# Kernel tuning notes

Hardware: AMD Instinct MI355X
Metric: run time of the kernel (lower is better)

Reference implementation:

```python
import jax, jax.numpy as jnp
import numpy as np
import math

EMB = 512

def setup_inputs() -> dict:
    key = jax.random.key(0)
    ks = jax.random.split(key, 7)
    B, L, E = 4, 4096, EMB
    s = 1.0 / math.sqrt(E)
    return {
        "x": jax.random.normal(ks[0], (B, L, E), dtype=jnp.float32),
        "Wq": jax.random.normal(ks[1], (E, E), dtype=jnp.float32) * s,
        "bq": jax.random.normal(ks[2], (E,), dtype=jnp.float32) * 0.01,
        "Wk": jax.random.normal(ks[3], (E, E), dtype=jnp.float32) * s,
        "bk": jax.random.normal(ks[4], (E,), dtype=jnp.float32) * 0.01,
        "Wv": jax.random.normal(ks[5], (E, E), dtype=jnp.float32) * s,
        "bv": jax.random.normal(ks[6], (E,), dtype=jnp.float32) * 0.01,
    }

def reference(x, Wq, bq, Wk, bk, Wv, bv):
    # x: [B, L, E]; Linear weights stored torch-style [out, in]
    E = x.shape[-1]
    L = x.shape[1]
    q = jnp.einsum('ble,fe->blf', x, Wq) + bq
    k = jnp.einsum('ble,fe->blf', x, Wk) + bk
    v = jnp.einsum('ble,fe->blf', x, Wv) + bv
    qk = jnp.einsum('bqe,bke->bqk', q, k)  # [B, L, L]
    # causal mask: strict upper triangle filled with -1e9 BEFORE scaling (as in source)
    mask = jnp.triu(jnp.ones((L, L), dtype=bool), k=1)
    qk = jnp.where(mask, jnp.float32(-1e9), qk)
    att = jax.nn.softmax(qk / jnp.sqrt(jnp.float32(E)), axis=-1)
    return jnp.einsum('bqk,bke->bqe', att, v)
```

## Files before the change

### kernel.cpp

```cpp
#include <hip/hip_runtime.h>

typedef unsigned short u16;
typedef unsigned int u32;
typedef short bf16x8 __attribute__((ext_vector_type(8)));
typedef float f32x4 __attribute__((ext_vector_type(4)));
typedef u16 u16x8 __attribute__((ext_vector_type(8)));
typedef u16 u16x4 __attribute__((ext_vector_type(4)));

typedef const __attribute__((address_space(1))) u32* gas_ptr;
typedef __attribute__((address_space(3))) u32* las_ptr;

#define LQ   4096
#define EMB  512
#define NB   4
#define MROWS (NB * LQ)
#define QSCALE 0.04419417382415922f

__device__ __forceinline__ u16 f2bf(float f) {
  unsigned u = __builtin_bit_cast(unsigned, f);
  u += 0x7fffu + ((u >> 16) & 1u);
  return (u16)(u >> 16);
}
__device__ __forceinline__ float bf2f(u16 h) {
  unsigned u = ((unsigned)h) << 16;
  return __builtin_bit_cast(float, u);
}

__global__ void prep_w(const float* __restrict__ Wq, const float* __restrict__ bq,
                       const float* __restrict__ Wk, const float* __restrict__ bk,
                       const float* __restrict__ Wv, const float* __restrict__ bv,
                       u16* __restrict__ wqb, u16* __restrict__ wkb, u16* __restrict__ wvb,
                       float* __restrict__ bias) {
  int i = blockIdx.x * 256 + threadIdx.x;
  if (i < EMB * EMB) {
    wqb[i] = f2bf(Wq[i] * QSCALE);
    wkb[i] = f2bf(Wk[i]);
    wvb[i] = f2bf(Wv[i]);
  }
  if (i < EMB) {
    bias[i]           = bq[i] * QSCALE;
    bias[EMB + i]     = bk[i];
    bias[2 * EMB + i] = bv[i];
  }
}

__global__ void prep_x(const float* __restrict__ x, u16* __restrict__ xb) {
  int i = blockIdx.x * 256 + threadIdx.x;
  const float4* p = (const float4*)(x + (size_t)i * 8);
  float4 a = p[0], b = p[1];
  u16x8 o;
  o[0] = f2bf(a.x); o[1] = f2bf(a.y); o[2] = f2bf(a.z); o[3] = f2bf(a.w);
  o[4] = f2bf(b.x); o[5] = f2bf(b.y); o[6] = f2bf(b.z); o[7] = f2bf(b.w);
  *(u16x8*)(xb + (size_t)i * 8) = o;
}

__device__ __forceinline__ void gemm_tile_core(
    const u16* __restrict__ A, int lda,
    const u16* __restrict__ B, int ldb,
    int kIters, u16* ldsA, u16* ldsB,
    f32x4 acc[4][4], int tid, int lane, int wr, int wc)
{
  int wave = tid >> 6;
  for (int kb = 0; kb < kIters; ++kb) {
    const u16* ga = A + kb * 64;
    const u16* gb = B + kb * 64;
#pragma unroll
    for (int p = 0; p < 4; ++p) {
      int c = tid + p * 256;
      int row = c >> 3, hh = c & 7;
      int h = hh ^ (row & 7);
      const u16* sa = ga + (size_t)row * lda + h * 8;
      const u16* sb = gb + (size_t)row * ldb + h * 8;
      u16* la = ldsA + wave * 512 + p * 2048;
      u16* lb = ldsB + wave * 512 + p * 2048;
      __builtin_amdgcn_global_load_lds((gas_ptr)(const void*)sa, (las_ptr)(void*)la, 16, 0, 0);
      __builtin_amdgcn_global_load_lds((gas_ptr)(const void*)sb, (las_ptr)(void*)lb, 16, 0, 0);
    }
    __syncthreads();
#pragma unroll
    for (int s = 0; s < 2; ++s) {
      bf16x8 af[4], bfr[4];
#pragma unroll
      for (int m = 0; m < 4; ++m) {
        int row = wr * 64 + m * 16 + (lane & 15);
        int hh = (s * 4 + (lane >> 4)) ^ (row & 7);
        af[m] = *(const bf16x8*)(ldsA + row * 64 + hh * 8);
      }
#pragma unroll
      for (int n = 0; n < 4; ++n) {
        int row = wc * 64 + n * 16 + (lane & 15);
        int hh = (s * 4 + (lane >> 4)) ^ (row & 7);
        bfr[n] = *(const bf16x8*)(ldsB + row * 64 + hh * 8);
      }
#pragma unroll
      for (int m = 0; m < 4; ++m)
#pragma unroll
        for (int n = 0; n < 4; ++n)
          acc[m][n] = __builtin_amdgcn_mfma_f32_16x16x32_bf16(af[m], bfr[n], acc[m][n], 0, 0, 0);
    }
    __syncthreads();
  }
}

__global__ __launch_bounds__(256, 2) void k_qkv(
    const u16* __restrict__ xb,
    const u16* __restrict__ w0, const u16* __restrict__ w1, const u16* __restrict__ w2,
    const float* __restrict__ bias,
    u16* __restrict__ o0, u16* __restrict__ o1, u16* __restrict__ o2)
{
  __shared__ uint4 ldsraw[2048];
  u16* ldsA = (u16*)ldsraw;
  u16* ldsB = (u16*)(ldsraw + 1024);
  int bi = blockIdx.x;
  int which = bi >> 9;
  int t = bi & 511;
  int rt = t >> 2, ct = t & 3;
  const u16* W = (which == 0) ? w0 : (which == 1) ? w1 : w2;
  const float* bs = bias + which * EMB;
  int tid = threadIdx.x, lane = tid & 63, wave = tid >> 6;
  int wr = wave >> 1, wc = wave & 1;
  f32x4 acc[4][4];
#pragma unroll
  for (int m = 0; m < 4; ++m)
#pragma unroll
    for (int n = 0; n < 4; ++n) acc[m][n] = (f32x4)0.0f;

  gemm_tile_core(xb + (size_t)rt * 128 * EMB, EMB,
                 W + (size_t)ct * 128 * EMB, EMB, EMB / 64,
                 ldsA, ldsB, acc, tid, lane, wr, wc);

#pragma unroll
  for (int m = 0; m < 4; ++m)
#pragma unroll
    for (int n = 0; n < 4; ++n) {
      int row0 = rt * 128 + wr * 64 + m * 16 + ((lane >> 4) << 2);
      int col  = ct * 128 + wc * 64 + n * 16 + (lane & 15);
      float bv = bs[col];
      if (which < 2) {
        u16* out = (which == 0) ? o0 : o1;
#pragma unroll
        for (int r = 0; r < 4; ++r)
          out[(size_t)(row0 + r) * EMB + col] = f2bf(acc[m][n][r] + bv);
      } else {
        int b = row0 >> 12, l0 = row0 & (LQ - 1);
        u16x4 pk;
#pragma unroll
        for (int r = 0; r < 4; ++r) pk[r] = f2bf(acc[m][n][r] + bv);
        *(u16x4*)(o2 + ((size_t)(b * EMB + col)) * LQ + l0) = pk;
      }
    }
}

__global__ __launch_bounds__(256, 2) void k_qk(
    const u16* __restrict__ Q, const u16* __restrict__ K,
    u16* __restrict__ S, int bstart)
{
  __shared__ uint4 ldsraw[2048];
  u16* ldsA = (u16*)ldsraw;
  u16* ldsB = (u16*)(ldsraw + 1024);
  int t = blockIdx.x;
  int b_local = t / 528;
  int i = t - b_local * 528;
  int qi = (int)((sqrtf(8.f * (float)i + 1.f) - 1.f) * 0.5f);
  while ((qi + 1) * (qi + 2) / 2 <= i) ++qi;
  while (qi * (qi + 1) / 2 > i) --qi;
  int ki = i - qi * (qi + 1) / 2;
  int bg = bstart + b_local;

  int tid = threadIdx.x, lane = tid & 63, wave = tid >> 6;
  int wr = wave >> 1, wc = wave & 1;
  f32x4 acc[4][4];
#pragma unroll
  for (int m = 0; m < 4; ++m)
#pragma unroll
    for (int n = 0; n < 4; ++n) acc[m][n] = (f32x4)0.0f;

  gemm_tile_core(Q + ((size_t)bg * LQ + qi * 128) * EMB, EMB,
                 K + ((size_t)bg * LQ + ki * 128) * EMB, EMB, EMB / 64,
                 ldsA, ldsB, acc, tid, lane, wr, wc);

  u16* Sb = S + (size_t)b_local * LQ * LQ;
#pragma unroll
  for (int m = 0; m < 4; ++m)
#pragma unroll
    for (int n = 0; n < 4; ++n) {
      int row0 = qi * 128 + wr * 64 + m * 16 + ((lane >> 4) << 2);
      int col  = ki * 128 + wc * 64 + n * 16 + (lane & 15);
#pragma unroll
      for (int r = 0; r < 4; ++r) {
        int row = row0 + r;
        float v = (col > row) ? -1e9f : acc[m][n][r];
        Sb[(size_t)row * LQ + col] = f2bf(v);
      }
    }
}

__global__ __launch_bounds__(256) void k_softmax(u16* __restrict__ S)
{
  int rowb = blockIdx.x;
  int q = rowb & (LQ - 1);
  u16* sr = S + (size_t)rowb * LQ;
  int n = ((q >> 7) + 1) << 7;
  int tid = threadIdx.x;
  int lane = tid & 63, wave = tid >> 6;
  __shared__ float red[8];

  float v[16];
  float mx = -3.0e38f;
#pragma unroll
  for (int p = 0; p < 2; ++p) {
    int idx = (p * 256 + tid) * 8;
    if (idx < n) {
      u16x8 raw = *(const u16x8*)(sr + idx);
#pragma unroll
      for (int j = 0; j < 8; ++j) {
        float f = bf2f(raw[j]);
        v[p * 8 + j] = f;
        mx = fmaxf(mx, f);
      }
    }
  }
#pragma unroll
  for (int off = 32; off >= 1; off >>= 1) mx = fmaxf(mx, __shfl_xor(mx, off));
  if (lane == 0) red[wave] = mx;
  __syncthreads();
  if (tid == 0) red[4] = fmaxf(fmaxf(red[0], red[1]), fmaxf(red[2], red[3]));
  __syncthreads();
  mx = red[4];
  __syncthreads();

  float sum = 0.f;
#pragma unroll
  for (int p = 0; p < 2; ++p) {
    int idx = (p * 256 + tid) * 8;
    if (idx < n) {
#pragma unroll
      for (int j = 0; j < 8; ++j) {
        float e = __expf(v[p * 8 + j] - mx);
        v[p * 8 + j] = e;
        sum += e;
      }
    }
  }
#pragma unroll
  for (int off = 32; off >= 1; off >>= 1) sum += __shfl_xor(sum, off);
  if (lane == 0) red[wave] = sum;
  __syncthreads();
  if (tid == 0) red[4] = red[0] + red[1] + red[2] + red[3];
  __syncthreads();
  float inv = 1.0f / red[4];

#pragma unroll
  for (int p = 0; p < 2; ++p) {
    int idx = (p * 256 + tid) * 8;
    if (idx < n) {
      u16x8 o;
#pragma unroll
      for (int j = 0; j < 8; ++j) o[j] = f2bf(v[p * 8 + j] * inv);
      *(u16x8*)(sr + idx) = o;
    }
  }
}

__global__ __launch_bounds__(256, 2) void k_pv(
    const u16* __restrict__ P, const u16* __restrict__ Vt,
    float* __restrict__ out, int bstart, int bcount)
{
  __shared__ uint4 ldsraw[2048];
  u16* ldsA = (u16*)ldsraw;
  u16* ldsB = (u16*)(ldsraw + 1024);
  int bi = blockIdx.x;
  int per_rt = bcount * 4;
  int idx = bi / per_rt;
  int rem = bi % per_rt;
  int rt = (idx < 16) ? (31 - idx) : (idx - 16);
  int b_local = rem >> 2, ct = rem & 3;
  int bg = bstart + b_local;

  int tid = threadIdx.x, lane = tid & 63, wave = tid >> 6;
  int wr = wave >> 1, wc = wave & 1;
  f32x4 acc[4][4];
#pragma unroll
  for (int m = 0; m < 4; ++m)
#pragma unroll
    for (int n = 0; n < 4; ++n) acc[m][n] = (f32x4)0.0f;

  int kIters = (rt + 1) * 2;
  gemm_tile_core(P + (size_t)b_local * LQ * LQ + (size_t)rt * 128 * LQ, LQ,
                 Vt + ((size_t)bg * EMB + ct * 128) * LQ, LQ, kIters,
                 ldsA, ldsB, acc, tid, lane, wr, wc);

#pragma unroll
  for (int m = 0; m < 4; ++m)
#pragma unroll
    for (int n = 0; n < 4; ++n) {
      int row0 = rt * 128 + wr * 64 + m * 16 + ((lane >> 4) << 2);
      int col  = ct * 128 + wc * 64 + n * 16 + (lane & 15);
#pragma unroll
      for (int r = 0; r < 4; ++r)
        out[((size_t)bg * LQ + row0 + r) * EMB + col] = acc[m][n][r];
    }
}

extern "C" void kernel_launch(void* const* d_in, const int* in_sizes, int n_in,
                              void* d_out, int out_size, void* d_ws, size_t ws_size,
                              hipStream_t stream) {
  const float* x  = (const float*)d_in[0];
  const float* Wq = (const float*)d_in[1];
  const float* bq = (const float*)d_in[2];
  const float* Wk = (const float*)d_in[3];
  const float* bk = (const float*)d_in[4];
  const float* Wv = (const float*)d_in[5];
  const float* bv = (const float*)d_in[6];

  char* ws = (char*)d_ws;
  size_t off = 0;
  u16* xb  = (u16*)(ws + off); off += (size_t)MROWS * EMB * 2;
  u16* wqb = (u16*)(ws + off); off += (size_t)EMB * EMB * 2;
  u16* wkb = (u16*)(ws + off); off += (size_t)EMB * EMB * 2;
  u16* wvb = (u16*)(ws + off); off += (size_t)EMB * EMB * 2;
  float* bias = (float*)(ws + off); off += 3 * EMB * 4;
  off = (off + 255) & ~(size_t)255;
  u16* Qb  = (u16*)(ws + off); off += (size_t)MROWS * EMB * 2;
  u16* Kb  = (u16*)(ws + off); off += (size_t)MROWS * EMB * 2;
  u16* Vtb = (u16*)(ws + off); off += (size_t)MROWS * EMB * 2;
  size_t fixed = off;
  size_t s_full = (size_t)NB * LQ * LQ * 2;
  int bcap = (ws_size >= fixed + s_full) ? NB : 1;
  u16* Sb = (u16*)(ws + fixed);

  prep_w<<<(EMB * EMB + 255) / 256, 256, 0, stream>>>(Wq, bq, Wk, bk, Wv, bv,
                                                      wqb, wkb, wvb, bias);
  prep_x<<<(MROWS * EMB / 8) / 256, 256, 0, stream>>>(x, xb);

  k_qkv<<<1536, 256, 0, stream>>>(xb, wqb, wkb, wvb, bias, Qb, Kb, Vtb);

  for (int bs = 0; bs < NB; bs += bcap) {
    int bc = (bs + bcap <= NB) ? bcap : (NB - bs);
    k_qk<<<528 * bc, 256, 0, stream>>>(Qb, Kb, Sb, bs);
    k_softmax<<<bc * LQ, 256, 0, stream>>>(Sb);
    k_pv<<<32 * bc * 4, 256, 0, stream>>>(Sb, Vtb, (float*)d_out, bs, bc);
  }
}
```

Baseline: 211.9 us.

## Fuse softmax into PV GEMM with online rescaling and double-buffer LDS

Removes the separate softmax pass over S by computing an online (flash-style) softmax inside the PV kernel, reading raw scores from LDS, exponentiating, and feeding bf16 probabilities straight to MFMA with a lazy rescale threshold. The GEMM cores gain double-buffered LDS staging so global loads for the next k-block overlap with MFMA work, and one barrier per iteration is dropped. PV now uses 512-thread blocks with 128x256 tiles and longest-row-first ordering, which cuts the grid to 64 blocks per batch and risks lower occupancy and load imbalance in exchange for avoiding the S read/write round trip.

```diff
diff --git a/kernel.cpp b/kernel.cpp
--- a/kernel.cpp
+++ b/kernel.cpp
@@ -54,29 +54,36 @@
   *(u16x8*)(xb + (size_t)i * 8) = o;
 }
 
-__device__ __forceinline__ void gemm_tile_core(
+__device__ __forceinline__ void stage128_256t(const u16* g, int ld, u16* lds, int tid) {
+  int wave = tid >> 6;
+#pragma unroll
+  for (int p = 0; p < 4; ++p) {
+    int c = tid + p * 256;
+    int row = c >> 3, hh = c & 7;
+    int h = hh ^ (row & 7);
+    const u16* src = g + (size_t)row * ld + h * 8;
+    u16* dst = lds + wave * 512 + p * 2048;
+    __builtin_amdgcn_global_load_lds((gas_ptr)(const void*)src, (las_ptr)(void*)dst, 16, 0, 0);
+  }
+}
+
+__device__ __forceinline__ void gemm_core_db(
     const u16* __restrict__ A, int lda,
     const u16* __restrict__ B, int ldb,
-    int kIters, u16* ldsA, u16* ldsB,
+    int kIters, u16* lds,
     f32x4 acc[4][4], int tid, int lane, int wr, int wc)
 {
-  int wave = tid >> 6;
+  stage128_256t(A, lda, lds, tid);
+  stage128_256t(B, ldb, lds + 8192, tid);
   for (int kb = 0; kb < kIters; ++kb) {
-    const u16* ga = A + kb * 64;
-    const u16* gb = B + kb * 64;
-#pragma unroll
-    for (int p = 0; p < 4; ++p) {
-      int c = tid + p * 256;
-      int row = c >> 3, hh = c & 7;
-      int h = hh ^ (row & 7);
-      const u16* sa = ga + (size_t)row * lda + h * 8;
-      const u16* sb = gb + (size_t)row * ldb + h * 8;
-      u16* la = ldsA + wave * 512 + p * 2048;
-      u16* lb = ldsB + wave * 512 + p * 2048;
-      __builtin_amdgcn_global_load_lds((gas_ptr)(const void*)sa, (las_ptr)(void*)la, 16, 0, 0);
-      __builtin_amdgcn_global_load_lds((gas_ptr)(const void*)sb, (las_ptr)(void*)lb, 16, 0, 0);
-    }
+    u16* ldsA = lds + (kb & 1) * 16384;
+    u16* ldsB = ldsA + 8192;
     __syncthreads();
+    if (kb + 1 < kIters) {
+      u16* nA = lds + ((kb + 1) & 1) * 16384;
+      stage128_256t(A + (kb + 1) * 64, lda, nA, tid);
+      stage128_256t(B + (kb + 1) * 64, ldb, nA + 8192, tid);
+    }
 #pragma unroll
     for (int s = 0; s < 2; ++s) {
       bf16x8 af[4], bfr[4];
@@ -98,7 +105,6 @@
         for (int n = 0; n < 4; ++n)
           acc[m][n] = __builtin_amdgcn_mfma_f32_16x16x32_bf16(af[m], bfr[n], acc[m][n], 0, 0, 0);
     }
-    __syncthreads();
   }
 }
 
@@ -108,9 +114,7 @@
     const float* __restrict__ bias,
     u16* __restrict__ o0, u16* __restrict__ o1, u16* __restrict__ o2)
 {
-  __shared__ uint4 ldsraw[2048];
-  u16* ldsA = (u16*)ldsraw;
-  u16* ldsB = (u16*)(ldsraw + 1024);
+  __shared__ __align__(16) u16 lds[32768];
   int bi = blockIdx.x;
   int which = bi >> 9;
   int t = bi & 511;
@@ -125,9 +129,9 @@
 #pragma unroll
     for (int n = 0; n < 4; ++n) acc[m][n] = (f32x4)0.0f;
 
-  gemm_tile_core(xb + (size_t)rt * 128 * EMB, EMB,
-                 W + (size_t)ct * 128 * EMB, EMB, EMB / 64,
-                 ldsA, ldsB, acc, tid, lane, wr, wc);
+  gemm_core_db(xb + (size_t)rt * 128 * EMB, EMB,
+               W + (size_t)ct * 128 * EMB, EMB, EMB / 64,
+               lds, acc, tid, lane, wr, wc);
 
 #pragma unroll
   for (int m = 0; m < 4; ++m)
@@ -155,9 +159,7 @@
     const u16* __restrict__ Q, const u16* __restrict__ K,
     u16* __restrict__ S, int bstart)
 {
-  __shared__ uint4 ldsraw[2048];
-  u16* ldsA = (u16*)ldsraw;
-  u16* ldsB = (u16*)(ldsraw + 1024);
+  __shared__ __align__(16) u16 lds[32768];
   int t = blockIdx.x;
   int b_local = t / 528;
   int i = t - b_local * 528;
@@ -175,9 +177,9 @@
 #pragma unroll
     for (int n = 0; n < 4; ++n) acc[m][n] = (f32x4)0.0f;
 
-  gemm_tile_core(Q + ((size_t)bg * LQ + qi * 128) * EMB, EMB,
-                 K + ((size_t)bg * LQ + ki * 128) * EMB, EMB, EMB / 64,
-                 ldsA, ldsB, acc, tid, lane, wr, wc);
+  gemm_core_db(Q + ((size_t)bg * LQ + qi * 128) * EMB, EMB,
+               K + ((size_t)bg * LQ + ki * 128) * EMB, EMB, EMB / 64,
+               lds, acc, tid, lane, wr, wc);
 
   u16* Sb = S + (size_t)b_local * LQ * LQ;
 #pragma unroll
@@ -195,111 +197,164 @@
     }
 }
 
-__global__ __launch_bounds__(256) void k_softmax(u16* __restrict__ S)
-{
-  int rowb = blockIdx.x;
-  int q = rowb & (LQ - 1);
-  u16* sr = S + (size_t)rowb * LQ;
-  int n = ((q >> 7) + 1) << 7;
-  int tid = threadIdx.x;
-  int lane = tid & 63, wave = tid >> 6;
-  __shared__ float red[8];
-
-  float v[16];
-  float mx = -3.0e38f;
-#pragma unroll
-  for (int p = 0; p < 2; ++p) {
-    int idx = (p * 256 + tid) * 8;
-    if (idx < n) {
-      u16x8 raw = *(const u16x8*)(sr + idx);
-#pragma unroll
-      for (int j = 0; j < 8; ++j) {
-        float f = bf2f(raw[j]);
-        v[p * 8 + j] = f;
-        mx = fmaxf(mx, f);
-      }
-    }
-  }
-#pragma unroll
-  for (int off = 32; off >= 1; off >>= 1) mx = fmaxf(mx, __shfl_xor(mx, off));
-  if (lane == 0) red[wave] = mx;
-  __syncthreads();
-  if (tid == 0) red[4] = fmaxf(fmaxf(red[0], red[1]), fmaxf(red[2], red[3]));
-  __syncthreads();
-  mx = red[4];
-  __syncthreads();
-
-  float sum = 0.f;
-#pragma unroll
-  for (int p = 0; p < 2; ++p) {
-    int idx = (p * 256 + tid) * 8;
-    if (idx < n) {
-#pragma unroll
-      for (int j = 0; j < 8; ++j) {
-        float e = __expf(v[p * 8 + j] - mx);
-        v[p * 8 + j] = e;
-        sum += e;
-      }
-    }
-  }
-#pragma unroll
-  for (int off = 32; off >= 1; off >>= 1) sum += __shfl_xor(sum, off);
-  if (lane == 0) red[wave] = sum;
-  __syncthreads();
-  if (tid == 0) red[4] = red[0] + red[1] + red[2] + red[3];
-  __syncthreads();
-  float inv = 1.0f / red[4];
-
-#pragma unroll
-  for (int p = 0; p < 2; ++p) {
-    int idx = (p * 256 + tid) * 8;
-    if (idx < n) {
-      u16x8 o;
-#pragma unroll
-      for (int j = 0; j < 8; ++j) o[j] = f2bf(v[p * 8 + j] * inv);
-      *(u16x8*)(sr + idx) = o;
-    }
-  }
-}
-
-__global__ __launch_bounds__(256, 2) void k_pv(
-    const u16* __restrict__ P, const u16* __restrict__ Vt,
+__global__ __launch_bounds__(512, 2) void k_pv2(
+    const u16* __restrict__ S, const u16* __restrict__ Vt,
     float* __restrict__ out, int bstart, int bcount)
 {
-  __shared__ uint4 ldsraw[2048];
-  u16* ldsA = (u16*)ldsraw;
-  u16* ldsB = (u16*)(ldsraw + 1024);
+  __shared__ __align__(16) u16 lds[49152];
   int bi = blockIdx.x;
-  int per_rt = bcount * 4;
-  int idx = bi / per_rt;
-  int rem = bi % per_rt;
-  int rt = (idx < 16) ? (31 - idx) : (idx - 16);
-  int b_local = rem >> 2, ct = rem & 3;
+  int per = 2 * bcount;
+  int idx = bi / per;
+  int rem = bi - idx * per;
+  int rt = 31 - idx;
+  int ct = rem / bcount;
+  int b_local = rem - ct * bcount;
   int bg = bstart + b_local;
+  int kIters = 2 * (rt + 1);
+
+  const u16* Ap = S + ((size_t)b_local * LQ + rt * 128) * LQ;
+  const u16* Bp = Vt + ((size_t)bg * EMB + ct * 256) * LQ;
 
   int tid = threadIdx.x, lane = tid & 63, wave = tid >> 6;
   int wr = wave >> 1, wc = wave & 1;
-  f32x4 acc[4][4];
-#pragma unroll
-  for (int m = 0; m < 4; ++m)
-#pragma unroll
-    for (int n = 0; n < 4; ++n) acc[m][n] = (f32x4)0.0f;
-
-  int kIters = (rt + 1) * 2;
-  gemm_tile_core(P + (size_t)b_local * LQ * LQ + (size_t)rt * 128 * LQ, LQ,
-                 Vt + ((size_t)bg * EMB + ct * 128) * LQ, LQ, kIters,
-                 ldsA, ldsB, acc, tid, lane, wr, wc);
-
-#pragma unroll
-  for (int m = 0; m < 4; ++m)
-#pragma unroll
-    for (int n = 0; n < 4; ++n) {
-      int row0 = rt * 128 + wr * 64 + m * 16 + ((lane >> 4) << 2);
-      int col  = ct * 128 + wc * 64 + n * 16 + (lane & 15);
-#pragma unroll
-      for (int r = 0; r < 4; ++r)
-        out[((size_t)bg * LQ + row0 + r) * EMB + col] = acc[m][n][r];
-    }
+  int l15 = lane & 15, lhi = lane >> 4;
+
+  f32x4 acc[2][8];
+#pragma unroll
+  for (int m = 0; m < 2; ++m)
+#pragma unroll
+    for (int n = 0; n < 8; ++n) acc[m][n] = (f32x4)0.0f;
+  float mrun[2] = {-3.0e38f, -3.0e38f};
+  float lrun[2] = {0.f, 0.f};
+
+  {
+#pragma unroll
+    for (int p = 0; p < 2; ++p) {
+      int c = tid + p * 512;
+      int row = c >> 3, hh = c & 7;
+      int h = hh ^ (row & 7);
+      __builtin_amdgcn_global_load_lds((gas_ptr)(const void*)(Ap + (size_t)row * LQ + h * 8),
+                                       (las_ptr)(void*)(lds + wave * 512 + p * 4096), 16, 0, 0);
+    }
+#pragma unroll
+    for (int p = 0; p < 4; ++p) {
+      int c = tid + p * 512;
+      int row = c >> 3, hh = c & 7;
+      int h = hh ^ (row & 7);
+      __builtin_amdgcn_global_load_lds((gas_ptr)(const void*)(Bp + (size_t)row * LQ + h * 8),
+                                       (las_ptr)(void*)(lds + 8192 + wave * 512 + p * 4096), 16, 0, 0);
+    }
+  }
+
+  for (int kb = 0; kb < kIters; ++kb) {
+    u16* ldsA = lds + (kb & 1) * 24576;
+    u16* ldsB = ldsA + 8192;
+    __syncthreads();
+    if (kb + 1 < kIters) {
+      u16* nA = lds + ((kb + 1) & 1) * 24576;
+      const u16* ga = Ap + (kb + 1) * 64;
+      const u16* gb = Bp + (kb + 1) * 64;
+#pragma unroll
+      for (int p = 0; p < 2; ++p) {
+        int c = tid + p * 512;
+        int row = c >> 3, hh = c & 7;
+        int h = hh ^ (row & 7);
+        __builtin_amdgcn_global_load_lds((gas_ptr)(const void*)(ga + (size_t)row * LQ + h * 8),
+                                         (las_ptr)(void*)(nA + wave * 512 + p * 4096), 16, 0, 0);
+      }
+#pragma unroll
+      for (int p = 0; p < 4; ++p) {
+        int c = tid + p * 512;
+        int row = c >> 3, hh = c & 7;
+        int h = hh ^ (row & 7);
+        __builtin_amdgcn_global_load_lds((gas_ptr)(const void*)(gb + (size_t)row * LQ + h * 8),
+                                         (las_ptr)(void*)(nA + 8192 + wave * 512 + p * 4096), 16, 0, 0);
+      }
+    }
+
+    float sv[2][16];
+#pragma unroll
+    for (int m = 0; m < 2; ++m) {
+      int row = wr * 32 + m * 16 + l15;
+#pragma unroll
+      for (int s = 0; s < 2; ++s) {
+        int hh = (s * 4 + lhi) ^ (row & 7);
+        u16x8 raw = *(const u16x8*)(ldsA + row * 64 + hh * 8);
+#pragma unroll
+        for (int j = 0; j < 8; ++j) sv[m][s * 8 + j] = bf2f(raw[j]);
+      }
+    }
+    float tmax[2];
+#pragma unroll
+    for (int m = 0; m < 2; ++m) {
+      float tm = sv[m][0];
+#pragma unroll
+      for (int k = 1; k < 16; ++k) tm = fmaxf(tm, sv[m][k]);
+      tm = fmaxf(tm, __shfl_xor(tm, 16));
+      tm = fmaxf(tm, __shfl_xor(tm, 32));
+      tmax[m] = tm;
+    }
+    bool need = (tmax[0] > mrun[0] + 8.f) || (tmax[1] > mrun[1] + 8.f);
+    if (__any(need)) {
+#pragma unroll
+      for (int m = 0; m < 2; ++m) {
+        float mn = fmaxf(mrun[m], tmax[m]);
+        float f = __expf(mrun[m] - mn);
+        mrun[m] = mn;
+        lrun[m] *= f;
+#pragma unroll
+        for (int r = 0; r < 4; ++r) {
+          float fr = __shfl(f, lhi * 4 + r);
+#pragma unroll
+          for (int n = 0; n < 8; ++n) acc[m][n][r] *= fr;
+        }
+      }
+    }
+    u16x8 pf[2][2];
+#pragma unroll
+    for (int m = 0; m < 2; ++m) {
+      float ts = 0.f;
+#pragma unroll
+      for (int s = 0; s < 2; ++s)
+#pragma unroll
+        for (int j = 0; j < 8; ++j) {
+          float p = __expf(sv[m][s * 8 + j] - mrun[m]);
+          ts += p;
+          pf[m][s][j] = f2bf(p);
+        }
+      ts += __shfl_xor(ts, 16);
+      ts += __shfl_xor(ts, 32);
+      lrun[m] += ts;
+    }
+#pragma unroll
+    for (int s = 0; s < 2; ++s) {
+#pragma unroll
+      for (int n = 0; n < 8; ++n) {
+        int col = wc * 128 + n * 16 + l15;
+        int hh = (s * 4 + lhi) ^ (col & 7);
+        bf16x8 bv = *(const bf16x8*)(ldsB + col * 64 + hh * 8);
+#pragma unroll
+        for (int m = 0; m < 2; ++m)
+          acc[m][n] = __builtin_amdgcn_mfma_f32_16x16x32_bf16(
+              __builtin_bit_cast(bf16x8, pf[m][s]), bv, acc[m][n], 0, 0, 0);
+      }
+    }
+  }
+
+#pragma unroll
+  for (int m = 0; m < 2; ++m) {
+    float linv = 1.0f / lrun[m];
+#pragma unroll
+    for (int r = 0; r < 4; ++r) {
+      float fr = __shfl(linv, lhi * 4 + r);
+      int grow = rt * 128 + wr * 32 + m * 16 + lhi * 4 + r;
+#pragma unroll
+      for (int n = 0; n < 8; ++n) {
+        int col = ct * 256 + wc * 128 + n * 16 + l15;
+        out[((size_t)bg * LQ + grow) * EMB + col] = acc[m][n][r] * fr;
+      }
+    }
+  }
 }
 
 extern "C" void kernel_launch(void* const* d_in, const int* in_sizes, int n_in,
@@ -338,7 +393,6 @@
   for (int bs = 0; bs < NB; bs += bcap) {
     int bc = (bs + bcap <= NB) ? bcap : (NB - bs);
     k_qk<<<528 * bc, 256, 0, stream>>>(Qb, Kb, Sb, bs);
-    k_softmax<<<bc * LQ, 256, 0, stream>>>(Sb);
-    k_pv<<<32 * bc * 4, 256, 0, stream>>>(Sb, Vtb, (float*)d_out, bs, bc);
-  }
-}
+    k_pv2<<<64 * bc, 512, 0, stream>>>(Sb, Vtb, (float*)d_out, bs, bc);
+  }
+}
```

New measurement: 257.2 us. 21.4% more time.
